# Performance work log

Measured on AMD Instinct MI355X. Metric: run time of the kernel, lower is better.

The kernel has to match this reference:

```python
import jax, jax.numpy as jnp
import numpy as np

N_COL, N_CON, E = 100000, 20000, 800000
D_COL, D_CON, H = 16, 8, 128


def _segment_mean(msgs, dst_idx, n_dst):
    # sum then divide by in-degree (0-degree nodes get 0, matching PyG scatter-mean)
    s = jax.ops.segment_sum(msgs, dst_idx, num_segments=n_dst)
    cnt = jax.ops.segment_sum(jnp.ones((dst_idx.shape[0], 1), msgs.dtype), dst_idx, num_segments=n_dst)
    return s / jnp.maximum(cnt, 1.0)


def _sage(x_src, x_dst, src_idx, dst_idx, Wl, bl, Wr):
    # PyG SAGEConv(mean): lin_l(mean_j x_j) + lin_r(x_i); lin_r has no bias
    agg = _segment_mean(x_src[src_idx], dst_idx, x_dst.shape[0])
    return agg @ Wl.T + bl + x_dst @ Wr.T


def setup_inputs():
    key = jax.random.key(0)
    ks = jax.random.split(key, 24)
    rn = lambda k, shape, s=0.05: jax.random.normal(k, shape, jnp.float32) * s
    z = lambda shape: jnp.zeros(shape, jnp.float32)
    inp = {
        'x_col': jax.random.normal(ks[0], (N_COL, D_COL), jnp.float32),
        'x_con': jax.random.normal(ks[1], (N_CON, D_CON), jnp.float32),
        'edge_col': jax.random.randint(ks[2], (E,), 0, N_COL, jnp.int32),
        'edge_con': jax.random.randint(ks[3], (E,), 0, N_CON, jnp.int32),
        'W_col': rn(ks[4], (H, D_COL)), 'b_col': z((H,)),
        'W_con': rn(ks[5], (H, D_CON)), 'b_con': z((H,)),
        'c1_cn_Wl': rn(ks[6], (H, H)), 'c1_cn_bl': z((H,)), 'c1_cn_Wr': rn(ks[7], (H, H)),
        'c1_nc_Wl': rn(ks[8], (H, H)), 'c1_nc_bl': z((H,)), 'c1_nc_Wr': rn(ks[9], (H, H)),
        'c2_cn_Wl': rn(ks[10], (H, H)), 'c2_cn_bl': z((H,)), 'c2_cn_Wr': rn(ks[11], (H, H)),
        'c2_nc_Wl': rn(ks[12], (H, H)), 'c2_nc_bl': z((H,)), 'c2_nc_Wr': rn(ks[13], (H, H)),
        'q_W1': rn(ks[14], (H // 2, H)), 'q_b1': z((H // 2,)),
        'q_W2': rn(ks[15], (1, H // 2)), 'q_b2': z((1,)),
    }
    return inp


def reference(x_col, x_con, edge_col, edge_con,
              W_col, b_col, W_con, b_con,
              c1_cn_Wl, c1_cn_bl, c1_cn_Wr, c1_nc_Wl, c1_nc_bl, c1_nc_Wr,
              c2_cn_Wl, c2_cn_bl, c2_cn_Wr, c2_nc_Wl, c2_nc_bl, c2_nc_Wr,
              q_W1, q_b1, q_W2, q_b2):
    relu = jax.nn.relu
    h_col = relu(x_col @ W_col.T + b_col)  # [N_COL, H]
    h_con = relu(x_con @ W_con.T + b_con)  # [N_CON, H]
    # conv1: 'serves' col->con, 'served_by' con->col (reverse edges)
    n_con = relu(_sage(h_col, h_con, edge_col, edge_con, c1_cn_Wl, c1_cn_bl, c1_cn_Wr))
    n_col = relu(_sage(h_con, h_col, edge_con, edge_col, c1_nc_Wl, c1_nc_bl, c1_nc_Wr))
    # conv2
    h_con2 = relu(_sage(n_col, n_con, edge_col, edge_con, c2_cn_Wl, c2_cn_bl, c2_cn_Wr))
    h_col2 = relu(_sage(n_con, n_col, edge_con, edge_col, c2_nc_Wl, c2_nc_bl, c2_nc_Wr))
    del h_con2  # constraint embeddings unused for Q-head
    q = relu(h_col2 @ q_W1.T + q_b1) @ q_W2.T + q_b2  # [N_COL, 1]
    return q[:, 0]
```

## Files before the change

kernel.cpp:

```cpp
#include <hip/hip_runtime.h>

#define N_COL 100000
#define N_CON 20000
#define HDIM 128
#define SCAN_B 1024

__global__ void transpose_k(const float* __restrict__ src, float* __restrict__ dst, int R, int C) {
    int idx = blockIdx.x * blockDim.x + threadIdx.x;
    if (idx < R * C) {
        int r = idx / C, c = idx - r * C;
        dst[c * R + r] = src[idx];
    }
}

template <int D>
__global__ __launch_bounds__(256) void encoder_k(const float* __restrict__ x,
                                                 const float* __restrict__ WT,
                                                 const float* __restrict__ b,
                                                 float* __restrict__ out, int N) {
    int idx = blockIdx.x * blockDim.x + threadIdx.x;
    if (idx >= N * HDIM) return;
    int n = idx >> 7, h = idx & 127;
    const float* xr = x + (size_t)n * D;
    float acc = b[h];
#pragma unroll
    for (int k = 0; k < D; k++) acc = fmaf(xr[k], WT[k * HDIM + h], acc);
    out[idx] = fmaxf(acc, 0.f);
}

__global__ void count_k(const int* __restrict__ ecol, const int* __restrict__ econ,
                        int* cnt_col, int* cnt_con, int E) {
    int e = blockIdx.x * blockDim.x + threadIdx.x;
    if (e < E) {
        atomicAdd(&cnt_col[ecol[e]], 1);
        atomicAdd(&cnt_con[econ[e]], 1);
    }
}

__global__ __launch_bounds__(256) void scan1_k(const int* __restrict__ cnt, int n,
                                               int* __restrict__ offs, int* __restrict__ partials) {
    __shared__ int lds[256];
    int t = threadIdx.x;
    int base = blockIdx.x * SCAN_B + t * 4;
    int v[4], s = 0;
#pragma unroll
    for (int i = 0; i < 4; i++) { int idx = base + i; v[i] = (idx < n) ? cnt[idx] : 0; s += v[i]; }
    lds[t] = s; __syncthreads();
    for (int off = 1; off < 256; off <<= 1) {
        int x = (t >= off) ? lds[t - off] : 0; __syncthreads();
        lds[t] += x; __syncthreads();
    }
    int excl = lds[t] - s;
    if (t == 255) partials[blockIdx.x] = lds[255];
    int run = excl;
#pragma unroll
    for (int i = 0; i < 4; i++) { int idx = base + i; if (idx < n) offs[idx] = run; run += v[i]; }
}

__global__ __launch_bounds__(256) void scan2_k(int* partials, int nb) {
    __shared__ int lds[256];
    int t = threadIdx.x;
    int v = (t < nb) ? partials[t] : 0;
    lds[t] = v; __syncthreads();
    for (int off = 1; off < 256; off <<= 1) {
        int x = (t >= off) ? lds[t - off] : 0; __syncthreads();
        lds[t] += x; __syncthreads();
    }
    if (t < nb) partials[t] = lds[t] - v;
}

__global__ void scan3_k(int* offs, int n, const int* __restrict__ partials) {
    int i = blockIdx.x * blockDim.x + threadIdx.x;
    if (i < n) offs[i] += partials[i / SCAN_B];
}

__global__ void fill_k(const int* __restrict__ sidx, const int* __restrict__ didx,
                       const int* __restrict__ offs, int* cursor, int* __restrict__ srclist, int E) {
    int e = blockIdx.x * blockDim.x + threadIdx.x;
    if (e < E) {
        int d = didx[e];
        int p = offs[d] + atomicAdd(&cursor[d], 1);
        srclist[p] = sidx[e];
    }
}

__global__ __launch_bounds__(256) void gather_mean_k(const float* __restrict__ tab,
                                                     const int* __restrict__ srclist,
                                                     const int* __restrict__ offs,
                                                     const int* __restrict__ cnt,
                                                     float* __restrict__ out, int N) {
    int wid = threadIdx.x >> 6, lane = threadIdx.x & 63;
    int n = blockIdx.x * 4 + wid;
    if (n >= N) return;
    int c = cnt[n], st = offs[n];
    const int* sl = srclist + st;
    int half = lane >> 5, q = (lane & 31) * 4;
    float ax = 0.f, ay = 0.f, az = 0.f, aw = 0.f;
    int j = 0;
    for (; j + 1 < c; j += 2) {
        int s = sl[j + half];
        float4 a = *reinterpret_cast<const float4*>(tab + (size_t)s * HDIM + q);
        ax += a.x; ay += a.y; az += a.z; aw += a.w;
    }
    if (j < c && half == 0) {
        int s = sl[j];
        float4 a = *reinterpret_cast<const float4*>(tab + (size_t)s * HDIM + q);
        ax += a.x; ay += a.y; az += a.z; aw += a.w;
    }
    ax += __shfl_xor(ax, 32); ay += __shfl_xor(ay, 32);
    az += __shfl_xor(az, 32); aw += __shfl_xor(aw, 32);
    if (half == 0) {
        float inv = 1.f / fmaxf((float)c, 1.f);
        float4 r; r.x = ax * inv; r.y = ay * inv; r.z = az * inv; r.w = aw * inv;
        *reinterpret_cast<float4*>(out + (size_t)n * HDIM + q) = r;
    }
}

__device__ __forceinline__ void gemm_core(float (*As)[36], float (*Ws)[132],
                                          const float* __restrict__ src,
                                          const float* __restrict__ W,
                                          int n0, int N, int t, float acc[4][8]) {
    int tx = t & 15, ty = t >> 4;
    int ar = t >> 2, akq = (t & 3) * 8;
    int wk = t >> 3, wc = (t & 7) * 16;
    for (int kb = 0; kb < 4; ++kb) {
        int k0 = kb * 32;
        {
            int row = n0 + ar;
            float4 v0 = make_float4(0.f, 0.f, 0.f, 0.f), v1 = v0;
            if (row < N) {
                const float* ap = src + (size_t)row * HDIM + k0 + akq;
                v0 = *reinterpret_cast<const float4*>(ap);
                v1 = *reinterpret_cast<const float4*>(ap + 4);
            }
            *reinterpret_cast<float4*>(&As[ar][akq]) = v0;
            *reinterpret_cast<float4*>(&As[ar][akq + 4]) = v1;
        }
        {
            const float* wp = W + (size_t)(k0 + wk) * HDIM + wc;
#pragma unroll
            for (int jj = 0; jj < 4; jj++)
                *reinterpret_cast<float4*>(&Ws[wk][wc + 4 * jj]) =
                    *reinterpret_cast<const float4*>(wp + 4 * jj);
        }
        __syncthreads();
#pragma unroll
        for (int k4 = 0; k4 < 8; ++k4) {
            float4 av[4];
#pragma unroll
            for (int i = 0; i < 4; i++)
                av[i] = *reinterpret_cast<const float4*>(&As[ty * 4 + i][k4 * 4]);
#pragma unroll
            for (int kk = 0; kk < 4; kk++) {
                float4 w0 = *reinterpret_cast<const float4*>(&Ws[k4 * 4 + kk][tx * 4]);
                float4 w1 = *reinterpret_cast<const float4*>(&Ws[k4 * 4 + kk][64 + tx * 4]);
                float w[8] = {w0.x, w0.y, w0.z, w0.w, w1.x, w1.y, w1.z, w1.w};
#pragma unroll
                for (int i = 0; i < 4; i++) {
                    float avk = (kk == 0) ? av[i].x : (kk == 1) ? av[i].y
                                : (kk == 2) ? av[i].z : av[i].w;
#pragma unroll
                    for (int j = 0; j < 8; j++) acc[i][j] = fmaf(avk, w[j], acc[i][j]);
                }
            }
        }
        __syncthreads();
    }
}

__device__ __forceinline__ void gemm_core_h(float (*Ha)[132], float (*Ws)[132],
                                            const float* __restrict__ W,
                                            int t, float acc[4][8]) {
    int tx = t & 15, ty = t >> 4;
    int wk = t >> 3, wc = (t & 7) * 16;
    for (int kb = 0; kb < 4; ++kb) {
        int k0 = kb * 32;
        {
            const float* wp = W + (size_t)(k0 + wk) * HDIM + wc;
#pragma unroll
            for (int jj = 0; jj < 4; jj++)
                *reinterpret_cast<float4*>(&Ws[wk][wc + 4 * jj]) =
                    *reinterpret_cast<const float4*>(wp + 4 * jj);
        }
        __syncthreads();
#pragma unroll
        for (int k4 = 0; k4 < 8; ++k4) {
            float4 av[4];
#pragma unroll
            for (int i = 0; i < 4; i++)
                av[i] = *reinterpret_cast<const float4*>(&Ha[ty * 4 + i][k0 + k4 * 4]);
#pragma unroll
            for (int kk = 0; kk < 4; kk++) {
                float4 w0 = *reinterpret_cast<const float4*>(&Ws[k4 * 4 + kk][tx * 4]);
                float4 w1 = *reinterpret_cast<const float4*>(&Ws[k4 * 4 + kk][64 + tx * 4]);
                float w[8] = {w0.x, w0.y, w0.z, w0.w, w1.x, w1.y, w1.z, w1.w};
#pragma unroll
                for (int i = 0; i < 4; i++) {
                    float avk = (kk == 0) ? av[i].x : (kk == 1) ? av[i].y
                                : (kk == 2) ? av[i].z : av[i].w;
#pragma unroll
                    for (int j = 0; j < 8; j++) acc[i][j] = fmaf(avk, w[j], acc[i][j]);
                }
            }
        }
        __syncthreads();
    }
}

__global__ __launch_bounds__(256) void lin_k(const float* __restrict__ src,
                                             const float* __restrict__ WT,
                                             float* __restrict__ out, int N) {
    __shared__ __align__(16) float As[64][36];
    __shared__ __align__(16) float Ws[32][132];
    int t = threadIdx.x;
    int tx = t & 15, ty = t >> 4;
    int n0 = blockIdx.x * 64;
    float acc[4][8];
#pragma unroll
    for (int i = 0; i < 4; i++)
#pragma unroll
        for (int j = 0; j < 8; j++) acc[i][j] = 0.f;
    gemm_core(As, Ws, src, WT, n0, N, t, acc);
#pragma unroll
    for (int i = 0; i < 4; i++) {
        int row = n0 + ty * 4 + i;
        if (row < N) {
            float* op = out + (size_t)row * HDIM;
            *reinterpret_cast<float4*>(op + tx * 4) = make_float4(acc[i][0], acc[i][1], acc[i][2], acc[i][3]);
            *reinterpret_cast<float4*>(op + 64 + tx * 4) = make_float4(acc[i][4], acc[i][5], acc[i][6], acc[i][7]);
        }
    }
}

__global__ __launch_bounds__(256) void sage_gemm_k(const float* __restrict__ agg,
                                                   const float* __restrict__ xdst,
                                                   const float* __restrict__ WlT,
                                                   const float* __restrict__ bl,
                                                   const float* __restrict__ WrT,
                                                   float* __restrict__ out, int N) {
    __shared__ __align__(16) float As[64][36];
    __shared__ __align__(16) float Ws[32][132];
    int t = threadIdx.x;
    int tx = t & 15, ty = t >> 4;
    int n0 = blockIdx.x * 64;
    float acc[4][8];
#pragma unroll
    for (int i = 0; i < 4; i++)
#pragma unroll
        for (int j = 0; j < 8; j++) acc[i][j] = 0.f;
    gemm_core(As, Ws, agg, WlT, n0, N, t, acc);
    gemm_core(As, Ws, xdst, WrT, n0, N, t, acc);
    float4 b0 = *reinterpret_cast<const float4*>(bl + tx * 4);
    float4 b1 = *reinterpret_cast<const float4*>(bl + 64 + tx * 4);
    float bb[8] = {b0.x, b0.y, b0.z, b0.w, b1.x, b1.y, b1.z, b1.w};
#pragma unroll
    for (int i = 0; i < 4; i++) {
        int row = n0 + ty * 4 + i;
        if (row < N) {
            float4 r0, r1;
            r0.x = fmaxf(acc[i][0] + bb[0], 0.f);
            r0.y = fmaxf(acc[i][1] + bb[1], 0.f);
            r0.z = fmaxf(acc[i][2] + bb[2], 0.f);
            r0.w = fmaxf(acc[i][3] + bb[3], 0.f);
            r1.x = fmaxf(acc[i][4] + bb[4], 0.f);
            r1.y = fmaxf(acc[i][5] + bb[5], 0.f);
            r1.z = fmaxf(acc[i][6] + bb[6], 0.f);
            r1.w = fmaxf(acc[i][7] + bb[7], 0.f);
            float* op = out + (size_t)row * HDIM;
            *reinterpret_cast<float4*>(op + tx * 4) = r0;
            *reinterpret_cast<float4*>(op + 64 + tx * 4) = r1;
        }
    }
}

__global__ __launch_bounds__(256) void col_mega_k(const float* __restrict__ c0_1,
                                                  const float* __restrict__ c0_2,
                                                  const float* __restrict__ xdst,
                                                  const float* __restrict__ Wr1T,
                                                  const float* __restrict__ bl1,
                                                  const float* __restrict__ Wr2T,
                                                  const float* __restrict__ bl2,
                                                  const float* __restrict__ W1T,
                                                  const float* __restrict__ b1v,
                                                  const float* __restrict__ W2,
                                                  const float* __restrict__ b2,
                                                  float* __restrict__ out, int N) {
    __shared__ __align__(16) char smem[59904];
    float (*H)[132] = reinterpret_cast<float(*)[132]>(smem);
    float (*As)[36] = reinterpret_cast<float(*)[36]>(smem + 33792);
    float (*Ws)[132] = reinterpret_cast<float(*)[132]>(smem + 43008);
    int t = threadIdx.x;
    int tx = t & 15, ty = t >> 4;
    int n0 = blockIdx.x * 64;
    float acc[4][8];
#pragma unroll
    for (int i = 0; i < 4; i++)
#pragma unroll
        for (int j = 0; j < 8; j++) acc[i][j] = 0.f;

    gemm_core(As, Ws, xdst, Wr1T, n0, N, t, acc);
    {
        float4 b0 = *reinterpret_cast<const float4*>(bl1 + tx * 4);
        float4 b1 = *reinterpret_cast<const float4*>(bl1 + 64 + tx * 4);
        float bb[8] = {b0.x, b0.y, b0.z, b0.w, b1.x, b1.y, b1.z, b1.w};
#pragma unroll
        for (int i = 0; i < 4; i++) {
            int row = n0 + ty * 4 + i;
            float4 ca = make_float4(0.f, 0.f, 0.f, 0.f), cb = ca;
            if (row < N) {
                const float* cp = c0_1 + (size_t)row * HDIM;
                ca = *reinterpret_cast<const float4*>(cp + tx * 4);
                cb = *reinterpret_cast<const float4*>(cp + 64 + tx * 4);
            }
            float* hp = &H[ty * 4 + i][0];
            *reinterpret_cast<float4*>(hp + tx * 4) = make_float4(
                fmaxf(acc[i][0] + ca.x + bb[0], 0.f), fmaxf(acc[i][1] + ca.y + bb[1], 0.f),
                fmaxf(acc[i][2] + ca.z + bb[2], 0.f), fmaxf(acc[i][3] + ca.w + bb[3], 0.f));
            *reinterpret_cast<float4*>(hp + 64 + tx * 4) = make_float4(
                fmaxf(acc[i][4] + cb.x + bb[4], 0.f), fmaxf(acc[i][5] + cb.y + bb[5], 0.f),
                fmaxf(acc[i][6] + cb.z + bb[6], 0.f), fmaxf(acc[i][7] + cb.w + bb[7], 0.f));
        }
    }
    __syncthreads();

#pragma unroll
    for (int i = 0; i < 4; i++)
#pragma unroll
        for (int j = 0; j < 8; j++) acc[i][j] = 0.f;
    gemm_core_h(H, Ws, Wr2T, t, acc);
    {
        float4 b0 = *reinterpret_cast<const float4*>(bl2 + tx * 4);
        float4 b1 = *reinterpret_cast<const float4*>(bl2 + 64 + tx * 4);
        float bb[8] = {b0.x, b0.y, b0.z, b0.w, b1.x, b1.y, b1.z, b1.w};
#pragma unroll
        for (int i = 0; i < 4; i++) {
            int row = n0 + ty * 4 + i;
            float4 ca = make_float4(0.f, 0.f, 0.f, 0.f), cb = ca;
            if (row < N) {
                const float* cp = c0_2 + (size_t)row * HDIM;
                ca = *reinterpret_cast<const float4*>(cp + tx * 4);
                cb = *reinterpret_cast<const float4*>(cp + 64 + tx * 4);
            }
            float* hp = &H[ty * 4 + i][0];
            *reinterpret_cast<float4*>(hp + tx * 4) = make_float4(
                fmaxf(acc[i][0] + ca.x + bb[0], 0.f), fmaxf(acc[i][1] + ca.y + bb[1], 0.f),
                fmaxf(acc[i][2] + ca.z + bb[2], 0.f), fmaxf(acc[i][3] + ca.w + bb[3], 0.f));
            *reinterpret_cast<float4*>(hp + 64 + tx * 4) = make_float4(
                fmaxf(acc[i][4] + cb.x + bb[4], 0.f), fmaxf(acc[i][5] + cb.y + bb[5], 0.f),
                fmaxf(acc[i][6] + cb.z + bb[6], 0.f), fmaxf(acc[i][7] + cb.w + bb[7], 0.f));
        }
    }
    __syncthreads();

    int tx2 = t & 7, ty2 = t >> 3;
    float acc2[2][8];
#pragma unroll
    for (int i = 0; i < 2; i++)
#pragma unroll
        for (int j = 0; j < 8; j++) acc2[i][j] = 0.f;
    for (int k4 = 0; k4 < HDIM / 4; ++k4) {
        float4 a0 = *reinterpret_cast<const float4*>(&H[ty2 * 2 + 0][k4 * 4]);
        float4 a1 = *reinterpret_cast<const float4*>(&H[ty2 * 2 + 1][k4 * 4]);
        float a[2][4] = {{a0.x, a0.y, a0.z, a0.w}, {a1.x, a1.y, a1.z, a1.w}};
#pragma unroll
        for (int kk = 0; kk < 4; kk++) {
            const float* wp = W1T + (size_t)(k4 * 4 + kk) * 64 + tx2 * 8;
            float4 w0 = *reinterpret_cast<const float4*>(wp);
            float4 w1 = *reinterpret_cast<const float4*>(wp + 4);
            float w[8] = {w0.x, w0.y, w0.z, w0.w, w1.x, w1.y, w1.z, w1.w};
#pragma unroll
            for (int i = 0; i < 2; i++)
#pragma unroll
                for (int j = 0; j < 8; j++) acc2[i][j] = fmaf(a[i][kk], w[j], acc2[i][j]);
        }
    }
    {
        float4 c0v = *reinterpret_cast<const float4*>(b1v + tx2 * 8);
        float4 c1v = *reinterpret_cast<const float4*>(b1v + tx2 * 8 + 4);
        float bb1[8] = {c0v.x, c0v.y, c0v.z, c0v.w, c1v.x, c1v.y, c1v.z, c1v.w};
        float4 d0 = *reinterpret_cast<const float4*>(W2 + tx2 * 8);
        float4 d1 = *reinterpret_cast<const float4*>(W2 + tx2 * 8 + 4);
        float w2[8] = {d0.x, d0.y, d0.z, d0.w, d1.x, d1.y, d1.z, d1.w};
#pragma unroll
        for (int i = 0; i < 2; i++) {
            float v = 0.f;
#pragma unroll
            for (int j = 0; j < 8; j++) v = fmaf(fmaxf(acc2[i][j] + bb1[j], 0.f), w2[j], v);
            v += __shfl_xor(v, 1);
            v += __shfl_xor(v, 2);
            v += __shfl_xor(v, 4);
            int row = n0 + ty2 * 2 + i;
            if (tx2 == 0 && row < N) out[row] = v + b2[0];
        }
    }
}

extern "C" void kernel_launch(void* const* d_in, const int* in_sizes, int n_in,
                              void* d_out, int out_size, void* d_ws, size_t ws_size,
                              hipStream_t stream) {
    const float* x_col = (const float*)d_in[0];
    const float* x_con = (const float*)d_in[1];
    const int* edge_col = (const int*)d_in[2];
    const int* edge_con = (const int*)d_in[3];
    const float* W_col = (const float*)d_in[4];
    const float* b_col = (const float*)d_in[5];
    const float* W_con = (const float*)d_in[6];
    const float* b_con = (const float*)d_in[7];
    const float* c1_cn_Wl = (const float*)d_in[8];
    const float* c1_cn_bl = (const float*)d_in[9];
    const float* c1_cn_Wr = (const float*)d_in[10];
    const float* c1_nc_Wl = (const float*)d_in[11];
    const float* c1_nc_bl = (const float*)d_in[12];
    const float* c1_nc_Wr = (const float*)d_in[13];
    const float* c2_nc_Wl = (const float*)d_in[17];
    const float* c2_nc_bl = (const float*)d_in[18];
    const float* c2_nc_Wr = (const float*)d_in[19];
    const float* q_W1 = (const float*)d_in[20];
    const float* q_b1 = (const float*)d_in[21];
    const float* q_W2 = (const float*)d_in[22];
    const float* q_b2 = (const float*)d_in[23];
    float* out = (float*)d_out;
    const int E = in_sizes[2];

    float* ws = (float*)d_ws;
    size_t o = 0;
    float* h_col = ws + o;   o += (size_t)N_COL * HDIM;
    float* h_con = ws + o;   o += (size_t)N_CON * HDIM;
    float* n_con = ws + o;   o += (size_t)N_CON * HDIM;
    float* c01 = ws + o;     o += (size_t)N_COL * HDIM;
    float* c02 = ws + o;     o += (size_t)N_COL * HDIM;
    float* bufB = ws + o;    o += (size_t)N_CON * HDIM;
    float* W_colT = ws + o;  o += 16 * HDIM;
    float* W_conT = ws + o;  o += 8 * HDIM;
    float* c1_cn_WlT = ws + o; o += HDIM * HDIM;
    float* c1_cn_WrT = ws + o; o += HDIM * HDIM;
    float* c1_nc_WlT = ws + o; o += HDIM * HDIM;
    float* c1_nc_WrT = ws + o; o += HDIM * HDIM;
    float* c2_nc_WlT = ws + o; o += HDIM * HDIM;
    float* c2_nc_WrT = ws + o; o += HDIM * HDIM;
    float* q_W1T = ws + o;     o += HDIM * 64;
    int* iws = (int*)(ws + o);
    size_t io = 0;
    int* cnt_col = iws + io;  io += N_COL;
    int* cnt_con = iws + io;  io += N_CON;
    int* offs_col = iws + io; io += N_COL;
    int* offs_con = iws + io; io += N_CON;
    int* cursor = iws + io;   io += N_COL;
    int* partials = iws + io; io += 256;
    int* srclist_col = iws + io; io += E;
    int* srclist_con = iws + io; io += E;

    auto T = [&](const float* s, float* d, int R, int C) {
        transpose_k<<<(R * C + 255) / 256, 256, 0, stream>>>(s, d, R, C);
    };
    T(W_col, W_colT, HDIM, 16);
    T(W_con, W_conT, HDIM, 8);
    T(c1_cn_Wl, c1_cn_WlT, HDIM, HDIM);
    T(c1_cn_Wr, c1_cn_WrT, HDIM, HDIM);
    T(c1_nc_Wl, c1_nc_WlT, HDIM, HDIM);
    T(c1_nc_Wr, c1_nc_WrT, HDIM, HDIM);
    T(c2_nc_Wl, c2_nc_WlT, HDIM, HDIM);
    T(c2_nc_Wr, c2_nc_WrT, HDIM, HDIM);
    T(q_W1, q_W1T, 64, HDIM);

    encoder_k<16><<<((size_t)N_COL * HDIM + 255) / 256, 256, 0, stream>>>(x_col, W_colT, b_col, h_col, N_COL);
    encoder_k<8><<<((size_t)N_CON * HDIM + 255) / 256, 256, 0, stream>>>(x_con, W_conT, b_con, h_con, N_CON);

    hipMemsetAsync(cnt_col, 0, (N_COL + N_CON) * sizeof(int), stream);
    count_k<<<(E + 255) / 256, 256, 0, stream>>>(edge_col, edge_con, cnt_col, cnt_con, E);

    int nb_col = (N_COL + SCAN_B - 1) / SCAN_B;
    int nb_con = (N_CON + SCAN_B - 1) / SCAN_B;
    scan1_k<<<nb_col, 256, 0, stream>>>(cnt_col, N_COL, offs_col, partials);
    scan2_k<<<1, 256, 0, stream>>>(partials, nb_col);
    scan3_k<<<(N_COL + 255) / 256, 256, 0, stream>>>(offs_col, N_COL, partials);
    scan1_k<<<nb_con, 256, 0, stream>>>(cnt_con, N_CON, offs_con, partials);
    scan2_k<<<1, 256, 0, stream>>>(partials, nb_con);
    scan3_k<<<(N_CON + 255) / 256, 256, 0, stream>>>(offs_con, N_CON, partials);

    hipMemsetAsync(cursor, 0, N_COL * sizeof(int), stream);
    fill_k<<<(E + 255) / 256, 256, 0, stream>>>(edge_con, edge_col, offs_col, cursor, srclist_col, E);
    hipMemsetAsync(cursor, 0, N_CON * sizeof(int), stream);
    fill_k<<<(E + 255) / 256, 256, 0, stream>>>(edge_col, edge_con, offs_con, cursor, srclist_con, E);

    gather_mean_k<<<(N_CON + 3) / 4, 256, 0, stream>>>(h_col, srclist_con, offs_con, cnt_con, bufB, N_CON);
    sage_gemm_k<<<(N_CON + 63) / 64, 256, 0, stream>>>(bufB, h_con, c1_cn_WlT, c1_cn_bl, c1_cn_WrT, n_con, N_CON);

    lin_k<<<(N_CON + 63) / 64, 256, 0, stream>>>(h_con, c1_nc_WlT, bufB, N_CON);
    gather_mean_k<<<(N_COL + 3) / 4, 256, 0, stream>>>(bufB, srclist_col, offs_col, cnt_col, c01, N_COL);
    lin_k<<<(N_CON + 63) / 64, 256, 0, stream>>>(n_con, c2_nc_WlT, bufB, N_CON);
    gather_mean_k<<<(N_COL + 3) / 4, 256, 0, stream>>>(bufB, srclist_col, offs_col, cnt_col, c02, N_COL);

    col_mega_k<<<(N_COL + 63) / 64, 256, 0, stream>>>(c01, c02, h_col,
                                                      c1_nc_WrT, c1_nc_bl, c2_nc_WrT, c2_nc_bl,
                                                      q_W1T, q_b1, q_W2, q_b2, out, N_COL);
}
```

Baseline: 763.1 us.

## Fuse dual col gathers into one kernel and stage xdst in shared memory

Replaces the two sequential gather-mean passes over the column adjacency with a single kernel. One half-wave gathers from each source table, so the index list, offsets and counts are read once and one launch is dropped. Both lin_k projections now run first, and h_con is reused as the second buffer. In col_mega_k the xdst tile is preloaded into the H shared buffer so the first GEMM can reuse gemm_core_h; this shrinks shared memory and removes a barrier. Correctness relies on gemm_core_h containing its own synchronisation around reads of H.

```diff
diff --git a/kernel.cpp b/kernel.cpp
--- a/kernel.cpp
+++ b/kernel.cpp
@@ -114,6 +114,39 @@
         float4 r; r.x = ax * inv; r.y = ay * inv; r.z = az * inv; r.w = aw * inv;
         *reinterpret_cast<float4*>(out + (size_t)n * HDIM + q) = r;
     }
+}
+
+__global__ __launch_bounds__(256) void gather_dual_k(const float* __restrict__ t1,
+                                                     const float* __restrict__ t2,
+                                                     const int* __restrict__ srclist,
+                                                     const int* __restrict__ offs,
+                                                     const int* __restrict__ cnt,
+                                                     float* __restrict__ o1,
+                                                     float* __restrict__ o2, int N) {
+    int wid = threadIdx.x >> 6, lane = threadIdx.x & 63;
+    int n = blockIdx.x * 4 + wid;
+    if (n >= N) return;
+    int c = cnt[n], st = offs[n];
+    const int* sl = srclist + st;
+    int half = lane >> 5, q = (lane & 31) * 4;
+    const float* tab = half ? t2 : t1;
+    float ax = 0.f, ay = 0.f, az = 0.f, aw = 0.f;
+    int j = 0;
+    for (; j + 1 < c; j += 2) {
+        int s0 = sl[j], s1 = sl[j + 1];
+        float4 a = *reinterpret_cast<const float4*>(tab + (size_t)s0 * HDIM + q);
+        float4 b = *reinterpret_cast<const float4*>(tab + (size_t)s1 * HDIM + q);
+        ax += a.x + b.x; ay += a.y + b.y; az += a.z + b.z; aw += a.w + b.w;
+    }
+    if (j < c) {
+        int s0 = sl[j];
+        float4 a = *reinterpret_cast<const float4*>(tab + (size_t)s0 * HDIM + q);
+        ax += a.x; ay += a.y; az += a.z; aw += a.w;
+    }
+    float inv = 1.f / fmaxf((float)c, 1.f);
+    float4 r; r.x = ax * inv; r.y = ay * inv; r.z = az * inv; r.w = aw * inv;
+    float* op = (half ? o2 : o1) + (size_t)n * HDIM + q;
+    *reinterpret_cast<float4*>(op) = r;
 }
 
 __device__ __forceinline__ void gemm_core(float (*As)[36], float (*Ws)[132],
@@ -285,20 +318,35 @@
                                                   const float* __restrict__ W2,
                                                   const float* __restrict__ b2,
                                                   float* __restrict__ out, int N) {
-    __shared__ __align__(16) char smem[59904];
+    __shared__ __align__(16) char smem[50688];
     float (*H)[132] = reinterpret_cast<float(*)[132]>(smem);
-    float (*As)[36] = reinterpret_cast<float(*)[36]>(smem + 33792);
-    float (*Ws)[132] = reinterpret_cast<float(*)[132]>(smem + 43008);
+    float (*Ws)[132] = reinterpret_cast<float(*)[132]>(smem + 33792);
     int t = threadIdx.x;
     int tx = t & 15, ty = t >> 4;
     int n0 = blockIdx.x * 64;
+
+    {
+        int xr = t >> 2, xc0 = (t & 3) * 32;
+        int row = n0 + xr;
+        if (row < N) {
+            const float* xp = xdst + (size_t)row * HDIM + xc0;
+#pragma unroll
+            for (int jj = 0; jj < 8; jj++)
+                *reinterpret_cast<float4*>(&H[xr][xc0 + 4 * jj]) =
+                    *reinterpret_cast<const float4*>(xp + 4 * jj);
+        } else {
+            float4 z = make_float4(0.f, 0.f, 0.f, 0.f);
+#pragma unroll
+            for (int jj = 0; jj < 8; jj++)
+                *reinterpret_cast<float4*>(&H[xr][xc0 + 4 * jj]) = z;
+        }
+    }
     float acc[4][8];
 #pragma unroll
     for (int i = 0; i < 4; i++)
 #pragma unroll
         for (int j = 0; j < 8; j++) acc[i][j] = 0.f;
-
-    gemm_core(As, Ws, xdst, Wr1T, n0, N, t, acc);
+    gemm_core_h(H, Ws, Wr1T, t, acc);
     {
         float4 b0 = *reinterpret_cast<const float4*>(bl1 + tx * 4);
         float4 b1 = *reinterpret_cast<const float4*>(bl1 + 64 + tx * 4);
@@ -321,8 +369,6 @@
                 fmaxf(acc[i][6] + cb.z + bb[6], 0.f), fmaxf(acc[i][7] + cb.w + bb[7], 0.f));
         }
     }
-    __syncthreads();
-
 #pragma unroll
     for (int i = 0; i < 4; i++)
 #pragma unroll
@@ -429,7 +475,7 @@
     float* n_con = ws + o;   o += (size_t)N_CON * HDIM;
     float* c01 = ws + o;     o += (size_t)N_COL * HDIM;
     float* c02 = ws + o;     o += (size_t)N_COL * HDIM;
-    float* bufB = ws + o;    o += (size_t)N_CON * HDIM;
+    float* buf1 = ws + o;    o += (size_t)N_CON * HDIM;
     float* W_colT = ws + o;  o += 16 * HDIM;
     float* W_conT = ws + o;  o += 8 * HDIM;
     float* c1_cn_WlT = ws + o; o += HDIM * HDIM;
@@ -449,6 +495,7 @@
     int* partials = iws + io; io += 256;
     int* srclist_col = iws + io; io += E;
     int* srclist_con = iws + io; io += E;
+    float* buf2 = h_con;
 
     auto T = [&](const float* s, float* d, int R, int C) {
         transpose_k<<<(R * C + 255) / 256, 256, 0, stream>>>(s, d, R, C);
@@ -483,13 +530,13 @@
     hipMemsetAsync(cursor, 0, N_CON * sizeof(int), stream);
     fill_k<<<(E + 255) / 256, 256, 0, stream>>>(edge_col, edge_con, offs_con, cursor, srclist_con, E);
 
-    gather_mean_k<<<(N_CON + 3) / 4, 256, 0, stream>>>(h_col, srclist_con, offs_con, cnt_con, bufB, N_CON);
-    sage_gemm_k<<<(N_CON + 63) / 64, 256, 0, stream>>>(bufB, h_con, c1_cn_WlT, c1_cn_bl, c1_cn_WrT, n_con, N_CON);
-
-    lin_k<<<(N_CON + 63) / 64, 256, 0, stream>>>(h_con, c1_nc_WlT, bufB, N_CON);
-    gather_mean_k<<<(N_COL + 3) / 4, 256, 0, stream>>>(bufB, srclist_col, offs_col, cnt_col, c01, N_COL);
-    lin_k<<<(N_CON + 63) / 64, 256, 0, stream>>>(n_con, c2_nc_WlT, bufB, N_CON);
-    gather_mean_k<<<(N_COL + 3) / 4, 256, 0, stream>>>(bufB, srclist_col, offs_col, cnt_col, c02, N_COL);
+    gather_mean_k<<<(N_CON + 3) / 4, 256, 0, stream>>>(h_col, srclist_con, offs_con, cnt_con, buf1, N_CON);
+    sage_gemm_k<<<(N_CON + 63) / 64, 256, 0, stream>>>(buf1, h_con, c1_cn_WlT, c1_cn_bl, c1_cn_WrT, n_con, N_CON);
+
+    lin_k<<<(N_CON + 63) / 64, 256, 0, stream>>>(h_con, c1_nc_WlT, buf1, N_CON);
+    lin_k<<<(N_CON + 63) / 64, 256, 0, stream>>>(n_con, c2_nc_WlT, buf2, N_CON);
+    gather_dual_k<<<(N_COL + 3) / 4, 256, 0, stream>>>(buf1, buf2, srclist_col, offs_col, cnt_col,
+                                                       c01, c02, N_COL);
 
     col_mega_k<<<(N_COL + 63) / 64, 256, 0, stream>>>(c01, c02, h_col,
                                                       c1_nc_WrT, c1_nc_bl, c2_nc_WrT, c2_nc_bl,
```

Measured after the change: 740.5 us. -3.0%, faster.
